# Performance work log

Hardware: AMD Instinct MI355X
Metric: run time of the kernel (lower is better)

The kernel has to match this reference:

```python
import jax, jax.numpy as jnp
import numpy as np
import math

H = 16
D_MODEL = 1024
D_K = D_MODEL // H


def setup_inputs() -> dict:
    key = jax.random.key(0)
    ks = jax.random.split(key, 12)
    B, S, D = 2, 2048, D_MODEL
    s = 1.0 / math.sqrt(D)
    inp = {
        "query": jax.random.normal(ks[0], (B, S, D), jnp.float32),
        "key": jax.random.normal(ks[1], (B, S, D), jnp.float32),
        "value": jax.random.normal(ks[2], (B, S, D), jnp.float32),
        "mask": jnp.ones((B, 1, S), jnp.int32),
        "wq": jax.random.normal(ks[3], (D, D), jnp.float32) * s,
        "bq": jnp.zeros((D,), jnp.float32),
        "wk": jax.random.normal(ks[4], (D, D), jnp.float32) * s,
        "bk": jnp.zeros((D,), jnp.float32),
        "wv": jax.random.normal(ks[5], (D, D), jnp.float32) * s,
        "bv": jnp.zeros((D,), jnp.float32),
        "wo": jax.random.normal(ks[6], (D, D), jnp.float32) * s,
        "bo": jnp.zeros((D,), jnp.float32),
    }
    return inp


def _split_heads(x, B, S):
    # [B, S, D] -> [B, H, S, D_K]
    return x.reshape(B, S, H, D_K).transpose(0, 2, 1, 3)


def reference(query, key, value, mask, wq, bq, wk, bk, wv, bv, wo, bo):
    B, S, D = query.shape
    q = _split_heads(query @ wq.T + bq, B, S)
    k = _split_heads(key @ wk.T + bk, B, S)
    v = _split_heads(value @ wv.T + bv, B, S)
    # scores: [B, H, S, S]
    scores = jnp.einsum("bhqd,bhkd->bhqk", q, k) / math.sqrt(D_K)
    m = mask[:, None, :, :]  # [B,1,1,S] after unsqueeze(1)
    scores = jnp.where(m == 0, jnp.float32(-1e9), scores)
    p_attn = jax.nn.softmax(scores, axis=-1)  # dropout = identity (eval)
    x = jnp.einsum("bhqk,bhkd->bhqd", p_attn, v)
    x = x.transpose(0, 2, 1, 3).reshape(B, S, D)
    return x @ wo.T + bo
```

## Files before the change

### kernel.cpp

```cpp
#include <hip/hip_runtime.h>
#include <hip/hip_bf16.h>

#define DEV __device__ __forceinline__

typedef __attribute__((ext_vector_type(8))) short bf16x8;
typedef __attribute__((ext_vector_type(4))) float f32x4;
typedef __attribute__((ext_vector_type(4))) unsigned u32x4;
typedef unsigned short u16;
typedef __attribute__((ext_vector_type(8))) unsigned short u16x8;

DEV u16 f2bf(float f) {
  union { float f; unsigned u; } v; v.f = f;
  unsigned r = v.u + 0x7fffu + ((v.u >> 16) & 1u);
  return (u16)(r >> 16);
}
DEV unsigned pack2(float a, float b) {
  return (unsigned)f2bf(a) | ((unsigned)f2bf(b) << 16);
}
DEV unsigned cvtpk(float a, float b) {
  unsigned r;
  asm("v_cvt_pk_bf16_f32 %0, %1, %2" : "=v"(r) : "v"(a), "v"(b));
  return r;
}

DEV void gl_lds16(const void* g, void* l) {
  __builtin_amdgcn_global_load_lds(
      (const __attribute__((address_space(1))) void*)g,
      (__attribute__((address_space(3))) void*)l, 16, 0, 0);
}

#define MFMA16(a, b, c) __builtin_amdgcn_mfma_f32_16x16x32_bf16((a), (b), (c), 0, 0, 0)

#define QSCALE 0.18033688011112042f

__global__ __launch_bounds__(256) void conv_all(
    const float* __restrict__ q, const float* __restrict__ k, const float* __restrict__ v,
    const float* __restrict__ wq, const float* __restrict__ wk,
    const float* __restrict__ wv, const float* __restrict__ wo,
    u16* __restrict__ dst)
{
  const long i = (long)(blockIdx.x * 256 + threadIdx.x) * 8;
  const float* src; long off;
  if      (i < 4194304)  { src = q;  off = i; }
  else if (i < 8388608)  { src = k;  off = i - 4194304; }
  else if (i < 12582912) { src = v;  off = i - 8388608; }
  else if (i < 13631488) { src = wq; off = i - 12582912; }
  else if (i < 14680064) { src = wk; off = i - 13631488; }
  else if (i < 15728640) { src = wv; off = i - 14680064; }
  else                   { src = wo; off = i - 15728640; }
  float4 a = *(const float4*)(src + off);
  float4 b = *(const float4*)(src + off + 4);
  u16x8 r;
  r[0] = f2bf(a.x); r[1] = f2bf(a.y); r[2] = f2bf(a.z); r[3] = f2bf(a.w);
  r[4] = f2bf(b.x); r[5] = f2bf(b.y); r[6] = f2bf(b.z); r[7] = f2bf(b.w);
  *(u16x8*)(dst + i) = r;
}

DEV void gemm_core(const u16* __restrict__ A, const u16* __restrict__ W,
                   u16* As, u16* Bs, int row0, int col0, f32x4 acc[4][4])
{
  const int tid  = threadIdx.x;
  const int wave = tid >> 6, lane = tid & 63;
  const int wm = wave >> 1, wn = wave & 1;
  const int lr = lane & 15, lk = lane >> 4;
  #pragma unroll 1
  for (int kt = 0; kt < 32; ++kt) {
    const int k0 = kt * 32;
    __syncthreads();
    #pragma unroll
    for (int i = 0; i < 2; ++i) {
      const int blk = i * 4 + wave;
      const int c = blk * 64 + lane;
      const int r = c >> 2, kc = (c & 3) * 8;
      gl_lds16(A + (row0 + r) * 1024 + k0 + kc, As + blk * 512 + lane * 8);
      gl_lds16(W + (col0 + r) * 1024 + k0 + kc, Bs + blk * 512 + lane * 8);
    }
    __syncthreads();
    bf16x8 a[4], b[4];
    #pragma unroll
    for (int m = 0; m < 4; ++m)
      a[m] = *(const bf16x8*)(As + (wm * 64 + m * 16 + lr) * 32 + lk * 8);
    #pragma unroll
    for (int n = 0; n < 4; ++n)
      b[n] = *(const bf16x8*)(Bs + (wn * 64 + n * 16 + lr) * 32 + lk * 8);
    __builtin_amdgcn_s_setprio(1);
    #pragma unroll
    for (int m = 0; m < 4; ++m)
      #pragma unroll
      for (int n = 0; n < 4; ++n)
        acc[m][n] = MFMA16(a[m], b[n], acc[m][n]);
    __builtin_amdgcn_s_setprio(0);
  }
}

__global__ __launch_bounds__(256, 3) void gemm_qkv(
    const u16* __restrict__ xq, const u16* __restrict__ xk, const u16* __restrict__ xv,
    const u16* __restrict__ wqb, const u16* __restrict__ wkb, const u16* __restrict__ wvb,
    const float* __restrict__ bq, const float* __restrict__ bk, const float* __restrict__ bv,
    u16* __restrict__ Qo, u16* __restrict__ Ko, u16* __restrict__ Vt)
{
  __shared__ u16 As[4096], Bs[4096];
  const int z = blockIdx.z;
  const u16* A = (z == 0) ? xq : (z == 1) ? xk : xv;
  const u16* W = (z == 0) ? wqb : (z == 1) ? wkb : wvb;
  const float* bias = (z == 0) ? bq : (z == 1) ? bk : bv;
  const int row0 = blockIdx.x * 128, col0 = blockIdx.y * 128;
  f32x4 acc[4][4] = {};
  gemm_core(A, W, As, Bs, row0, col0, acc);
  const int tid = threadIdx.x, wave = tid >> 6, lane = tid & 63;
  const int wm = wave >> 1, wn = wave & 1, lr = lane & 15, lq = lane >> 4;
  if (z < 2) {
    const float sc = (z == 0) ? QSCALE : 1.0f;
    u16* outp = (z == 0) ? Qo : Ko;
    #pragma unroll
    for (int m = 0; m < 4; ++m)
      #pragma unroll
      for (int n = 0; n < 4; ++n) {
        const int cc = col0 + wn * 64 + n * 16 + lr;
        const float bb = bias[cc];
        #pragma unroll
        for (int j = 0; j < 4; ++j) {
          const int rr = row0 + wm * 64 + m * 16 + lq * 4 + j;
          outp[rr * 1024 + cc] = f2bf((acc[m][n][j] + bb) * sc);
        }
      }
  } else {
    #pragma unroll
    for (int m = 0; m < 4; ++m)
      #pragma unroll
      for (int n = 0; n < 4; ++n) {
        const int cc = col0 + wn * 64 + n * 16 + lr;
        const float bb = bias[cc];
        const int h = cc >> 6, dk = cc & 63;
        #pragma unroll
        for (int j = 0; j < 4; ++j) {
          const int rr = row0 + wm * 64 + m * 16 + lq * 4 + j;
          const int b_ = rr >> 11, s_ = rr & 2047;
          Vt[(((b_ * 16 + h) * 64 + dk) << 11) + s_] = f2bf(acc[m][n][j] + bb);
        }
      }
  }
}

__global__ __launch_bounds__(256, 4) void flash(
    const u16* __restrict__ Q, const u16* __restrict__ K,
    const u16* __restrict__ Vt, const int* __restrict__ mask,
    u16* __restrict__ X)
{
  __shared__ u16 Ks[2][4096], Vs[2][4096];
  const int qt = blockIdx.x, bh = blockIdx.y;
  const int b = bh >> 4, h = bh & 15;
  const int tid = threadIdx.x, wave = tid >> 6, lane = tid & 63;
  const int lr = lane & 15, lq = lane >> 4;
  const int qbase = qt * 64 + wave * 16;

  const u16* Kg = K + (long)b * 2048 * 1024 + h * 64;
  const u16* Vg = Vt + (long)(b * 16 + h) * 64 * 2048;
  const int* mb = mask + b * 2048;

  const u16* Qrow = Q + (long)(b * 2048 + qbase + lr) * 1024 + h * 64 + lq * 8;
  const bf16x8 bq0 = *(const bf16x8*)Qrow;
  const bf16x8 bq1 = *(const bf16x8*)(Qrow + 32);

  const int r1  = tid >> 3;
  const int c41 = (tid & 7) ^ (r1 & 7);
  const long gK1 = (long)r1 * 1024 + c41 * 8;
  const long gV1 = (long)r1 * 2048 + c41 * 8;
  const int xv    = lq ^ (lr & 7);
  const int offLo = (lr * 8 + xv) * 8;
  const int offHi = (lr * 8 + (xv ^ 4)) * 8;

  float mrow = -1e30f, lsum = 0.f;
  f32x4 o[4] = {};

  gl_lds16(Kg + gK1,             &Ks[0][tid * 8]);
  gl_lds16(Kg + gK1 + 32 * 1024, &Ks[0][tid * 8 + 2048]);
  gl_lds16(Vg + gV1,             &Vs[0][tid * 8]);
  gl_lds16(Vg + gV1 + 32 * 2048, &Vs[0][tid * 8 + 2048]);
  __syncthreads();

  #pragma unroll 1
  for (int t = 0; t < 32; ++t) {
    const int cur = t & 1, nxt = cur ^ 1;
    const int kv0 = t * 64;
    if (t < 31) {
      const long kq = kv0 + 64;
      gl_lds16(Kg + kq * 1024 + gK1,        &Ks[nxt][tid * 8]);
      gl_lds16(Kg + (kq + 32) * 1024 + gK1, &Ks[nxt][tid * 8 + 2048]);
      gl_lds16(Vg + kq + gV1,               &Vs[nxt][tid * 8]);
      gl_lds16(Vg + kq + gV1 + 32 * 2048,   &Vs[nxt][tid * 8 + 2048]);
    }
    const u16* kb = Ks[cur];
    f32x4 st[4];
    __builtin_amdgcn_s_setprio(1);
    #pragma unroll
    for (int n = 0; n < 4; ++n) {
      const bf16x8 klo = *(const bf16x8*)(kb + n * 1024 + offLo);
      const bf16x8 khi = *(const bf16x8*)(kb + n * 1024 + offHi);
      f32x4 z = {};
      z = MFMA16(klo, bq0, z);
      z = MFMA16(khi, bq1, z);
      st[n] = z;
    }
    __builtin_amdgcn_s_setprio(0);
    const int mv = mb[kv0 + lane];
    if (!__all(mv != 0)) {
      #pragma unroll
      for (int n = 0; n < 4; ++n) {
        const int4 mm = *(const int4*)(mb + kv0 + n * 16 + lq * 4);
        st[n][0] = mm.x ? st[n][0] : -1e9f;
        st[n][1] = mm.y ? st[n][1] : -1e9f;
        st[n][2] = mm.z ? st[n][2] : -1e9f;
        st[n][3] = mm.w ? st[n][3] : -1e9f;
      }
    }
    float pm = st[0][0];
    #pragma unroll
    for (int n = 0; n < 4; ++n)
      #pragma unroll
      for (int j = 0; j < 4; ++j)
        pm = fmaxf(pm, st[n][j]);
    pm = fmaxf(pm, __shfl_xor(pm, 16, 64));
    pm = fmaxf(pm, __shfl_xor(pm, 32, 64));
    if (!__all(pm - mrow <= 8.0f)) {
      const float mn = fmaxf(mrow, pm);
      const float corr = __builtin_amdgcn_exp2f(mrow - mn);
      mrow = mn;
      lsum *= corr;
      #pragma unroll
      for (int n = 0; n < 4; ++n)
        #pragma unroll
        for (int j = 0; j < 4; ++j)
          o[n][j] *= corr;
    }
    float rs = 0.f;
    #pragma unroll
    for (int n = 0; n < 4; ++n)
      #pragma unroll
      for (int j = 0; j < 4; ++j) {
        st[n][j] = __builtin_amdgcn_exp2f(st[n][j] - mrow);
        rs += st[n][j];
      }
    rs += __shfl_xor(rs, 16, 64);
    rs += __shfl_xor(rs, 32, 64);
    lsum += rs;
    unsigned pk0[2], pk1[2], pk2[2], pk3[2];
    pk0[0] = cvtpk(st[0][0], st[0][1]); pk0[1] = cvtpk(st[0][2], st[0][3]);
    pk1[0] = cvtpk(st[1][0], st[1][1]); pk1[1] = cvtpk(st[1][2], st[1][3]);
    pk2[0] = cvtpk(st[2][0], st[2][1]); pk2[1] = cvtpk(st[2][2], st[2][3]);
    pk3[0] = cvtpk(st[3][0], st[3][1]); pk3[1] = cvtpk(st[3][2], st[3][3]);
    const int sl0 = lr + 32 * (lq & 1);
    const int sl1 = sl0 + 16;
    const bool hiN = (lq >> 1) != 0;
    u32x4 w0, w1;
    {
      const unsigned a0 = __shfl(pk0[0], sl0, 64), b0 = __shfl(pk1[0], sl0, 64);
      const unsigned a1 = __shfl(pk0[1], sl0, 64), b1 = __shfl(pk1[1], sl0, 64);
      const unsigned a2 = __shfl(pk0[0], sl1, 64), b2 = __shfl(pk1[0], sl1, 64);
      const unsigned a3 = __shfl(pk0[1], sl1, 64), b3 = __shfl(pk1[1], sl1, 64);
      w0[0] = hiN ? b0 : a0; w0[1] = hiN ? b1 : a1;
      w0[2] = hiN ? b2 : a2; w0[3] = hiN ? b3 : a3;
    }
    {
      const unsigned a0 = __shfl(pk2[0], sl0, 64), b0 = __shfl(pk3[0], sl0, 64);
      const unsigned a1 = __shfl(pk2[1], sl0, 64), b1 = __shfl(pk3[1], sl0, 64);
      const unsigned a2 = __shfl(pk2[0], sl1, 64), b2 = __shfl(pk3[0], sl1, 64);
      const unsigned a3 = __shfl(pk2[1], sl1, 64), b3 = __shfl(pk3[1], sl1, 64);
      w1[0] = hiN ? b0 : a0; w1[1] = hiN ? b1 : a1;
      w1[2] = hiN ? b2 : a2; w1[3] = hiN ? b3 : a3;
    }
    union { u32x4 u; bf16x8 h; } cb0, cb1;
    cb0.u = w0; cb1.u = w1;
    const u16* vb = Vs[cur];
    __builtin_amdgcn_s_setprio(1);
    #pragma unroll
    for (int n = 0; n < 4; ++n) {
      const bf16x8 vlo = *(const bf16x8*)(vb + n * 1024 + offLo);
      const bf16x8 vhi = *(const bf16x8*)(vb + n * 1024 + offHi);
      o[n] = MFMA16(vlo, cb0.h, o[n]);
      o[n] = MFMA16(vhi, cb1.h, o[n]);
    }
    __builtin_amdgcn_s_setprio(0);
    __syncthreads();
  }

  const float inv = 1.0f / lsum;
  const long xrow = (long)(b * 2048 + qbase + lr) * 1024 + h * 64;
  #pragma unroll
  for (int n = 0; n < 4; ++n) {
    *(unsigned*)(X + xrow + n * 16 + lq * 4)     = pack2(o[n][0] * inv, o[n][1] * inv);
    *(unsigned*)(X + xrow + n * 16 + lq * 4 + 2) = pack2(o[n][2] * inv, o[n][3] * inv);
  }
}

__global__ __launch_bounds__(256, 3) void gemm_out(
    const u16* __restrict__ X, const u16* __restrict__ Wo,
    const float* __restrict__ bo, float* __restrict__ out)
{
  __shared__ u16 As[4096], Bs[4096];
  const int row0 = blockIdx.x * 128, col0 = blockIdx.y * 128;
  f32x4 acc[4][4] = {};
  gemm_core(X, Wo, As, Bs, row0, col0, acc);
  const int tid = threadIdx.x, wave = tid >> 6, lane = tid & 63;
  const int wm = wave >> 1, wn = wave & 1, lr = lane & 15, lq = lane >> 4;
  #pragma unroll
  for (int m = 0; m < 4; ++m)
    #pragma unroll
    for (int n = 0; n < 4; ++n) {
      const int cc = col0 + wn * 64 + n * 16 + lr;
      const float bb = bo[cc];
      #pragma unroll
      for (int j = 0; j < 4; ++j) {
        const int rr = row0 + wm * 64 + m * 16 + lq * 4 + j;
        out[rr * 1024 + cc] = acc[m][n][j] + bb;
      }
    }
}

extern "C" void kernel_launch(void* const* d_in, const int* in_sizes, int n_in,
                              void* d_out, int out_size, void* d_ws, size_t ws_size,
                              hipStream_t stream) {
  const float* q   = (const float*)d_in[0];
  const float* k   = (const float*)d_in[1];
  const float* v   = (const float*)d_in[2];
  const int*   msk = (const int*)d_in[3];
  const float* wq  = (const float*)d_in[4];
  const float* bq  = (const float*)d_in[5];
  const float* wk  = (const float*)d_in[6];
  const float* bk  = (const float*)d_in[7];
  const float* wv  = (const float*)d_in[8];
  const float* bv  = (const float*)d_in[9];
  const float* wo  = (const float*)d_in[10];
  const float* bo  = (const float*)d_in[11];

  u16* ws  = (u16*)d_ws;
  u16* xq  = ws;
  u16* xk  = ws + 4194304;
  u16* xv  = ws + 8388608;
  u16* wqb = ws + 12582912;
  u16* wkb = ws + 13631488;
  u16* wvb = ws + 14680064;
  u16* wob = ws + 15728640;
  u16* Qb  = ws + 16777216;
  u16* Kb  = ws + 20971520;
  u16* Vtb = ws + 25165824;
  u16* Xb  = ws + 29360128;

  conv_all<<<8192, 256, 0, stream>>>(q, k, v, wq, wk, wv, wo, ws);
  gemm_qkv<<<dim3(32, 8, 3), 256, 0, stream>>>(xq, xk, xv, wqb, wkb, wvb,
                                               bq, bk, bv, Qb, Kb, Vtb);
  flash<<<dim3(32, 32), 256, 0, stream>>>(Qb, Kb, Vtb, msk, Xb);
  gemm_out<<<dim3(32, 8), 256, 0, stream>>>(Xb, wob, bo, (float*)d_out);
}
```

Before: 247.1 us.

## Give each flash wave two query tiles and vectorize V-transpose stores

The flash kernel now runs 128 threads (2 waves) per block, and each wave handles 32 query rows as two 16-row tiles. Each K/V fragment read from LDS feeds two MFMAs, which halves LDS reads per unit of compute, at the cost of more registers and fewer waves per block to hide latency. The tile loads are spread over 4 passes per thread to cover the same 64-row K/V tiles. Separately, the V-transpose epilogue in the projection GEMM packs four bf16 values with cvt_pk and writes them in one 8-byte store instead of four scalar stores. The final output conversion also switches to the hardware pack instruction.

```diff
diff --git a/kernel.cpp b/kernel.cpp
--- a/kernel.cpp
+++ b/kernel.cpp
@@ -13,9 +13,6 @@
   union { float f; unsigned u; } v; v.f = f;
   unsigned r = v.u + 0x7fffu + ((v.u >> 16) & 1u);
   return (u16)(r >> 16);
-}
-DEV unsigned pack2(float a, float b) {
-  return (unsigned)f2bf(a) | ((unsigned)f2bf(b) << 16);
 }
 DEV unsigned cvtpk(float a, float b) {
   unsigned r;
@@ -132,17 +129,17 @@
         const int cc = col0 + wn * 64 + n * 16 + lr;
         const float bb = bias[cc];
         const int h = cc >> 6, dk = cc & 63;
-        #pragma unroll
-        for (int j = 0; j < 4; ++j) {
-          const int rr = row0 + wm * 64 + m * 16 + lq * 4 + j;
-          const int b_ = rr >> 11, s_ = rr & 2047;
-          Vt[(((b_ * 16 + h) * 64 + dk) << 11) + s_] = f2bf(acc[m][n][j] + bb);
-        }
-      }
-  }
-}
-
-__global__ __launch_bounds__(256, 4) void flash(
+        const int rr = row0 + wm * 64 + m * 16 + lq * 4;
+        const int b_ = rr >> 11, s_ = rr & 2047;
+        uint2 pr;
+        pr.x = cvtpk(acc[m][n][0] + bb, acc[m][n][1] + bb);
+        pr.y = cvtpk(acc[m][n][2] + bb, acc[m][n][3] + bb);
+        *(uint2*)(Vt + (((long)(b_ * 16 + h) * 64 + dk) << 11) + s_) = pr;
+      }
+  }
+}
+
+__global__ __launch_bounds__(128, 2) void flash(
     const u16* __restrict__ Q, const u16* __restrict__ K,
     const u16* __restrict__ Vt, const int* __restrict__ mask,
     u16* __restrict__ X)
@@ -152,15 +149,18 @@
   const int b = bh >> 4, h = bh & 15;
   const int tid = threadIdx.x, wave = tid >> 6, lane = tid & 63;
   const int lr = lane & 15, lq = lane >> 4;
-  const int qbase = qt * 64 + wave * 16;
+  const int qbase = qt * 64 + wave * 32;
 
   const u16* Kg = K + (long)b * 2048 * 1024 + h * 64;
   const u16* Vg = Vt + (long)(b * 16 + h) * 64 * 2048;
   const int* mb = mask + b * 2048;
 
   const u16* Qrow = Q + (long)(b * 2048 + qbase + lr) * 1024 + h * 64 + lq * 8;
-  const bf16x8 bq0 = *(const bf16x8*)Qrow;
-  const bf16x8 bq1 = *(const bf16x8*)(Qrow + 32);
+  bf16x8 bq0[2], bq1[2];
+  bq0[0] = *(const bf16x8*)Qrow;
+  bq1[0] = *(const bf16x8*)(Qrow + 32);
+  bq0[1] = *(const bf16x8*)(Qrow + 16 * 1024);
+  bq1[1] = *(const bf16x8*)(Qrow + 16 * 1024 + 32);
 
   const int r1  = tid >> 3;
   const int c41 = (tid & 7) ^ (r1 & 7);
@@ -170,13 +170,14 @@
   const int offLo = (lr * 8 + xv) * 8;
   const int offHi = (lr * 8 + (xv ^ 4)) * 8;
 
-  float mrow = -1e30f, lsum = 0.f;
-  f32x4 o[4] = {};
-
-  gl_lds16(Kg + gK1,             &Ks[0][tid * 8]);
-  gl_lds16(Kg + gK1 + 32 * 1024, &Ks[0][tid * 8 + 2048]);
-  gl_lds16(Vg + gV1,             &Vs[0][tid * 8]);
-  gl_lds16(Vg + gV1 + 32 * 2048, &Vs[0][tid * 8 + 2048]);
+  float mrow[2] = {-1e30f, -1e30f}, lsum[2] = {0.f, 0.f};
+  f32x4 o[2][4] = {};
+
+  #pragma unroll
+  for (int p = 0; p < 4; ++p) {
+    gl_lds16(Kg + gK1 + (long)p * 16 * 1024, &Ks[0][tid * 8 + p * 1024]);
+    gl_lds16(Vg + gV1 + (long)p * 16 * 2048, &Vs[0][tid * 8 + p * 1024]);
+  }
   __syncthreads();
 
   #pragma unroll 1
@@ -184,23 +185,28 @@
     const int cur = t & 1, nxt = cur ^ 1;
     const int kv0 = t * 64;
     if (t < 31) {
-      const long kq = kv0 + 64;
-      gl_lds16(Kg + kq * 1024 + gK1,        &Ks[nxt][tid * 8]);
-      gl_lds16(Kg + (kq + 32) * 1024 + gK1, &Ks[nxt][tid * 8 + 2048]);
-      gl_lds16(Vg + kq + gV1,               &Vs[nxt][tid * 8]);
-      gl_lds16(Vg + kq + gV1 + 32 * 2048,   &Vs[nxt][tid * 8 + 2048]);
+      const u16* Kn = Kg + (long)(kv0 + 64) * 1024;
+      const u16* Vn = Vg + kv0 + 64;
+      #pragma unroll
+      for (int p = 0; p < 4; ++p) {
+        gl_lds16(Kn + gK1 + (long)p * 16 * 1024, &Ks[nxt][tid * 8 + p * 1024]);
+        gl_lds16(Vn + gV1 + (long)p * 16 * 2048, &Vs[nxt][tid * 8 + p * 1024]);
+      }
     }
     const u16* kb = Ks[cur];
-    f32x4 st[4];
+    f32x4 st[2][4];
     __builtin_amdgcn_s_setprio(1);
     #pragma unroll
     for (int n = 0; n < 4; ++n) {
       const bf16x8 klo = *(const bf16x8*)(kb + n * 1024 + offLo);
       const bf16x8 khi = *(const bf16x8*)(kb + n * 1024 + offHi);
-      f32x4 z = {};
-      z = MFMA16(klo, bq0, z);
-      z = MFMA16(khi, bq1, z);
-      st[n] = z;
+      #pragma unroll
+      for (int u = 0; u < 2; ++u) {
+        f32x4 z = {};
+        z = MFMA16(klo, bq0[u], z);
+        z = MFMA16(khi, bq1[u], z);
+        st[u][n] = z;
+      }
     }
     __builtin_amdgcn_s_setprio(0);
     const int mv = mb[kv0 + lane];
@@ -208,88 +214,100 @@
       #pragma unroll
       for (int n = 0; n < 4; ++n) {
         const int4 mm = *(const int4*)(mb + kv0 + n * 16 + lq * 4);
-        st[n][0] = mm.x ? st[n][0] : -1e9f;
-        st[n][1] = mm.y ? st[n][1] : -1e9f;
-        st[n][2] = mm.z ? st[n][2] : -1e9f;
-        st[n][3] = mm.w ? st[n][3] : -1e9f;
-      }
-    }
-    float pm = st[0][0];
-    #pragma unroll
-    for (int n = 0; n < 4; ++n)
-      #pragma unroll
-      for (int j = 0; j < 4; ++j)
-        pm = fmaxf(pm, st[n][j]);
-    pm = fmaxf(pm, __shfl_xor(pm, 16, 64));
-    pm = fmaxf(pm, __shfl_xor(pm, 32, 64));
-    if (!__all(pm - mrow <= 8.0f)) {
-      const float mn = fmaxf(mrow, pm);
-      const float corr = __builtin_amdgcn_exp2f(mrow - mn);
-      mrow = mn;
-      lsum *= corr;
+        #pragma unroll
+        for (int u = 0; u < 2; ++u) {
+          st[u][n][0] = mm.x ? st[u][n][0] : -1e9f;
+          st[u][n][1] = mm.y ? st[u][n][1] : -1e9f;
+          st[u][n][2] = mm.z ? st[u][n][2] : -1e9f;
+          st[u][n][3] = mm.w ? st[u][n][3] : -1e9f;
+        }
+      }
+    }
+    union { u32x4 u; bf16x8 h; } cb0[2], cb1[2];
+    #pragma unroll
+    for (int u = 0; u < 2; ++u) {
+      float pm = st[u][0][0];
       #pragma unroll
       for (int n = 0; n < 4; ++n)
         #pragma unroll
         for (int j = 0; j < 4; ++j)
-          o[n][j] *= corr;
-    }
-    float rs = 0.f;
-    #pragma unroll
-    for (int n = 0; n < 4; ++n)
-      #pragma unroll
-      for (int j = 0; j < 4; ++j) {
-        st[n][j] = __builtin_amdgcn_exp2f(st[n][j] - mrow);
-        rs += st[n][j];
-      }
-    rs += __shfl_xor(rs, 16, 64);
-    rs += __shfl_xor(rs, 32, 64);
-    lsum += rs;
-    unsigned pk0[2], pk1[2], pk2[2], pk3[2];
-    pk0[0] = cvtpk(st[0][0], st[0][1]); pk0[1] = cvtpk(st[0][2], st[0][3]);
-    pk1[0] = cvtpk(st[1][0], st[1][1]); pk1[1] = cvtpk(st[1][2], st[1][3]);
-    pk2[0] = cvtpk(st[2][0], st[2][1]); pk2[1] = cvtpk(st[2][2], st[2][3]);
-    pk3[0] = cvtpk(st[3][0], st[3][1]); pk3[1] = cvtpk(st[3][2], st[3][3]);
-    const int sl0 = lr + 32 * (lq & 1);
-    const int sl1 = sl0 + 16;
-    const bool hiN = (lq >> 1) != 0;
-    u32x4 w0, w1;
-    {
-      const unsigned a0 = __shfl(pk0[0], sl0, 64), b0 = __shfl(pk1[0], sl0, 64);
-      const unsigned a1 = __shfl(pk0[1], sl0, 64), b1 = __shfl(pk1[1], sl0, 64);
-      const unsigned a2 = __shfl(pk0[0], sl1, 64), b2 = __shfl(pk1[0], sl1, 64);
-      const unsigned a3 = __shfl(pk0[1], sl1, 64), b3 = __shfl(pk1[1], sl1, 64);
-      w0[0] = hiN ? b0 : a0; w0[1] = hiN ? b1 : a1;
-      w0[2] = hiN ? b2 : a2; w0[3] = hiN ? b3 : a3;
-    }
-    {
-      const unsigned a0 = __shfl(pk2[0], sl0, 64), b0 = __shfl(pk3[0], sl0, 64);
-      const unsigned a1 = __shfl(pk2[1], sl0, 64), b1 = __shfl(pk3[1], sl0, 64);
-      const unsigned a2 = __shfl(pk2[0], sl1, 64), b2 = __shfl(pk3[0], sl1, 64);
-      const unsigned a3 = __shfl(pk2[1], sl1, 64), b3 = __shfl(pk3[1], sl1, 64);
-      w1[0] = hiN ? b0 : a0; w1[1] = hiN ? b1 : a1;
-      w1[2] = hiN ? b2 : a2; w1[3] = hiN ? b3 : a3;
-    }
-    union { u32x4 u; bf16x8 h; } cb0, cb1;
-    cb0.u = w0; cb1.u = w1;
+          pm = fmaxf(pm, st[u][n][j]);
+      pm = fmaxf(pm, __shfl_xor(pm, 16, 64));
+      pm = fmaxf(pm, __shfl_xor(pm, 32, 64));
+      if (!__all(pm - mrow[u] <= 8.0f)) {
+        const float mn = fmaxf(mrow[u], pm);
+        const float corr = __builtin_amdgcn_exp2f(mrow[u] - mn);
+        mrow[u] = mn;
+        lsum[u] *= corr;
+        #pragma unroll
+        for (int n = 0; n < 4; ++n)
+          #pragma unroll
+          for (int j = 0; j < 4; ++j)
+            o[u][n][j] *= corr;
+      }
+      float rs = 0.f;
+      #pragma unroll
+      for (int n = 0; n < 4; ++n)
+        #pragma unroll
+        for (int j = 0; j < 4; ++j) {
+          st[u][n][j] = __builtin_amdgcn_exp2f(st[u][n][j] - mrow[u]);
+          rs += st[u][n][j];
+        }
+      rs += __shfl_xor(rs, 16, 64);
+      rs += __shfl_xor(rs, 32, 64);
+      lsum[u] += rs;
+      unsigned pk0[2], pk1[2], pk2[2], pk3[2];
+      pk0[0] = cvtpk(st[u][0][0], st[u][0][1]); pk0[1] = cvtpk(st[u][0][2], st[u][0][3]);
+      pk1[0] = cvtpk(st[u][1][0], st[u][1][1]); pk1[1] = cvtpk(st[u][1][2], st[u][1][3]);
+      pk2[0] = cvtpk(st[u][2][0], st[u][2][1]); pk2[1] = cvtpk(st[u][2][2], st[u][2][3]);
+      pk3[0] = cvtpk(st[u][3][0], st[u][3][1]); pk3[1] = cvtpk(st[u][3][2], st[u][3][3]);
+      const int sl0 = lr + 32 * (lq & 1);
+      const int sl1 = sl0 + 16;
+      const bool hiN = (lq >> 1) != 0;
+      u32x4 w0, w1;
+      {
+        const unsigned a0 = __shfl(pk0[0], sl0, 64), b0 = __shfl(pk1[0], sl0, 64);
+        const unsigned a1 = __shfl(pk0[1], sl0, 64), b1 = __shfl(pk1[1], sl0, 64);
+        const unsigned a2 = __shfl(pk0[0], sl1, 64), b2 = __shfl(pk1[0], sl1, 64);
+        const unsigned a3 = __shfl(pk0[1], sl1, 64), b3 = __shfl(pk1[1], sl1, 64);
+        w0[0] = hiN ? b0 : a0; w0[1] = hiN ? b1 : a1;
+        w0[2] = hiN ? b2 : a2; w0[3] = hiN ? b3 : a3;
+      }
+      {
+        const unsigned a0 = __shfl(pk2[0], sl0, 64), b0 = __shfl(pk3[0], sl0, 64);
+        const unsigned a1 = __shfl(pk2[1], sl0, 64), b1 = __shfl(pk3[1], sl0, 64);
+        const unsigned a2 = __shfl(pk2[0], sl1, 64), b2 = __shfl(pk3[0], sl1, 64);
+        const unsigned a3 = __shfl(pk2[1], sl1, 64), b3 = __shfl(pk3[1], sl1, 64);
+        w1[0] = hiN ? b0 : a0; w1[1] = hiN ? b1 : a1;
+        w1[2] = hiN ? b2 : a2; w1[3] = hiN ? b3 : a3;
+      }
+      cb0[u].u = w0; cb1[u].u = w1;
+    }
     const u16* vb = Vs[cur];
     __builtin_amdgcn_s_setprio(1);
     #pragma unroll
     for (int n = 0; n < 4; ++n) {
       const bf16x8 vlo = *(const bf16x8*)(vb + n * 1024 + offLo);
       const bf16x8 vhi = *(const bf16x8*)(vb + n * 1024 + offHi);
-      o[n] = MFMA16(vlo, cb0.h, o[n]);
-      o[n] = MFMA16(vhi, cb1.h, o[n]);
+      #pragma unroll
+      for (int u = 0; u < 2; ++u) {
+        o[u][n] = MFMA16(vlo, cb0[u].h, o[u][n]);
+        o[u][n] = MFMA16(vhi, cb1[u].h, o[u][n]);
+      }
     }
     __builtin_amdgcn_s_setprio(0);
     __syncthreads();
   }
 
-  const float inv = 1.0f / lsum;
-  const long xrow = (long)(b * 2048 + qbase + lr) * 1024 + h * 64;
   #pragma unroll
-  for (int n = 0; n < 4; ++n) {
-    *(unsigned*)(X + xrow + n * 16 + lq * 4)     = pack2(o[n][0] * inv, o[n][1] * inv);
-    *(unsigned*)(X + xrow + n * 16 + lq * 4 + 2) = pack2(o[n][2] * inv, o[n][3] * inv);
+  for (int u = 0; u < 2; ++u) {
+    const float inv = 1.0f / lsum[u];
+    const long xrow = (long)(b * 2048 + qbase + u * 16 + lr) * 1024 + h * 64;
+    #pragma unroll
+    for (int n = 0; n < 4; ++n) {
+      *(unsigned*)(X + xrow + n * 16 + lq * 4)     = cvtpk(o[u][n][0] * inv, o[u][n][1] * inv);
+      *(unsigned*)(X + xrow + n * 16 + lq * 4 + 2) = cvtpk(o[u][n][2] * inv, o[u][n][3] * inv);
+    }
   }
 }
 
@@ -349,6 +367,6 @@
   conv_all<<<8192, 256, 0, stream>>>(q, k, v, wq, wk, wv, wo, ws);
   gemm_qkv<<<dim3(32, 8, 3), 256, 0, stream>>>(xq, xk, xv, wqb, wkb, wvb,
                                                bq, bk, bv, Qb, Kb, Vtb);
-  flash<<<dim3(32, 32), 256, 0, stream>>>(Qb, Kb, Vtb, msk, Xb);
+  flash<<<dim3(32, 32), 128, 0, stream>>>(Qb, Kb, Vtb, msk, Xb);
   gemm_out<<<dim3(32, 8), 256, 0, stream>>>(Xb, wob, bo, (float*)d_out);
 }
```

Measured after the change: 259.4 us. +5.0%, slower.
